# Kernel tuning notes

Hardware: AMD Instinct MI355X
Metric: run time of the kernel (lower is better)

## Reference

```python
import jax, jax.numpy as jnp
import numpy as np

NUM_HEADS = 16
KV_CHANNELS = 128
MASK_FILL = -10000.0  # TE attention_mask_func fill value


def setup_inputs() -> dict:
    key = jax.random.key(0)
    k1, k2, k3 = jax.random.split(key, 3)
    S, B, H = 2048, 2, 2048
    hidden_states = jax.random.normal(k1, (S, B, H), dtype=jnp.float32)
    attention_mask = jnp.zeros((B, 1, S, S), dtype=bool)  # True = masked out
    qkv_weight = jax.random.normal(k2, (H, 3 * H), dtype=jnp.float32) * (1.0 / np.sqrt(H))
    qkv_bias = jnp.zeros((3 * H,), dtype=jnp.float32)
    proj_weight = jax.random.normal(k3, (H, H), dtype=jnp.float32) * (1.0 / np.sqrt(H))
    proj_bias = jnp.zeros((H,), dtype=jnp.float32)
    return {
        "hidden_states": hidden_states,
        "attention_mask": attention_mask,
        "qkv_weight": qkv_weight,
        "qkv_bias": qkv_bias,
        "proj_weight": proj_weight,
        "proj_bias": proj_bias,
    }


def reference(hidden_states, attention_mask, qkv_weight, qkv_bias, proj_weight, proj_bias):
    S, B, H = hidden_states.shape
    nh, d = NUM_HEADS, KV_CHANNELS
    # QKV GEMM: [s,b,H] @ [H,3H] -> [s,b,3H] -> [s,b,nh,3d] -> split
    mixed = hidden_states @ qkv_weight + qkv_bias
    mixed = mixed.reshape(S, B, nh, 3 * d)
    q, k, v = jnp.split(mixed, 3, axis=-1)  # each [s,b,nh,d]
    # BMM1 with 1/sqrt(d) scaling (layer_number=None -> no layer scaling)
    norm_factor = jnp.asarray(np.sqrt(d), dtype=hidden_states.dtype)
    scores = jnp.einsum("sbhd,tbhd->bhst", q, k) / norm_factor  # [b,nh,s,s]
    # causal mask (future positions masked) OR'd with provided bool padding mask
    causal = ~jnp.tril(jnp.ones((S, S), dtype=bool))  # True above diagonal
    mask = jnp.logical_or(causal[None, None], attention_mask)
    scores = jnp.where(mask, jnp.asarray(MASK_FILL, scores.dtype), scores)
    probs = jax.nn.softmax(scores, axis=-1)
    # dropout is identity in eval mode (training=False)
    # BMM2: [b,nh,s,t] x [t,b,nh,d] -> [s,b,nh,d] -> [s,b,H]
    context = jnp.einsum("bhst,tbhd->sbhd", probs, v).reshape(S, B, H)
    # output projection; TE Dense(use_bias=False, return_bias=True) returns bias
    out = context @ proj_weight
    return out, proj_bias
```

## Files before the change

kernel.cpp:

```cpp
#include <hip/hip_runtime.h>
#include <cstdint>
#include <math.h>

#define S_LEN 2048
#define BATCH 2
#define HID   2048
#define NHEAD 16
#define DHEAD 128

typedef _Float16 h8 __attribute__((ext_vector_type(8)));
typedef _Float16 h4 __attribute__((ext_vector_type(4)));
typedef float f32x4 __attribute__((ext_vector_type(4)));

__device__ __forceinline__ void gload16(const void* g, void* l) {
  __builtin_amdgcn_global_load_lds(
      (const __attribute__((address_space(1))) unsigned int*)g,
      (__attribute__((address_space(3))) unsigned int*)l, 16, 0, 0);
}

template <bool HAS_BIAS, bool OUT_HALF>
__global__ __launch_bounds__(512) void gemm_128(
    const _Float16* __restrict__ A, const _Float16* __restrict__ Bt,
    const float* __restrict__ bias, void* __restrict__ Cout, int M, int N,
    int K) {
  __shared__ _Float16 LA[2][8192];
  __shared__ _Float16 LB[2][16384];
  const int tid = (int)threadIdx.x;
  const int wave = tid >> 6, lane = tid & 63;
  const int ln = lane & 15, quad = lane >> 4;
  const int wm = wave >> 2, wn = wave & 3;
  const int bm = (int)blockIdx.y * 128, bn = (int)blockIdx.x * 256;
  const int NT = K >> 6;

  const int gc8 = ((lane & 7) ^ (lane >> 3)) * 8;
  const uint32_t oA0 =
      (uint32_t)(bm + wave * 8 + (lane >> 3)) * (uint32_t)K + (uint32_t)gc8;
  const uint32_t oA1 = oA0 + (uint32_t)(64 * K);
  const uint32_t oB00 =
      (uint32_t)(bn + wave * 16 + (lane >> 3)) * (uint32_t)K + (uint32_t)gc8;
  const uint32_t oB01 = oB00 + (uint32_t)(8 * K);
  const uint32_t oB10 = oB00 + (uint32_t)(128 * K);
  const uint32_t oB11 = oB10 + (uint32_t)(8 * K);

#define STAGE128(bb_, u_)                                                    \
  {                                                                          \
    gload16(A + (oA0 + (uint32_t)(u_)*64u), &LA[bb_][wave * 512]);           \
    gload16(A + (oA1 + (uint32_t)(u_)*64u), &LA[bb_][4096 + wave * 512]);    \
    gload16(Bt + (oB00 + (uint32_t)(u_)*64u), &LB[bb_][wave * 1024]);        \
    gload16(Bt + (oB01 + (uint32_t)(u_)*64u), &LB[bb_][wave * 1024 + 512]);  \
    gload16(Bt + (oB10 + (uint32_t)(u_)*64u), &LB[bb_][8192 + wave * 1024]); \
    gload16(Bt + (oB11 + (uint32_t)(u_)*64u),                                \
            &LB[bb_][8192 + wave * 1024 + 512]);                             \
  }

  const int arow = ln * 64;
  const int sc0 = ((quad ^ (ln & 7))) * 8;
  const int sc1 = (((4 + quad) ^ (ln & 7))) * 8;
  const int abase = wm * 4096;
  const int bbase = wn * 4096;

  f32x4 acc[4][4];
#pragma unroll
  for (int m = 0; m < 4; m++)
#pragma unroll
    for (int n = 0; n < 4; n++) acc[m][n] = (f32x4){0.f, 0.f, 0.f, 0.f};
  h8 aF[4][2], bF[4][2];

#define HQUAD(n0_)                                                           \
  _Pragma("unroll") for (int mm_ = 0; mm_ < 4; mm_++)                        \
      _Pragma("unroll") for (int nn_ = 0; nn_ < 2; nn_++) {                  \
    acc[mm_][(n0_) + nn_] = __builtin_amdgcn_mfma_f32_16x16x32_f16(          \
        aF[mm_][0], bF[(n0_) + nn_][0], acc[mm_][(n0_) + nn_], 0, 0, 0);     \
    acc[mm_][(n0_) + nn_] = __builtin_amdgcn_mfma_f32_16x16x32_f16(          \
        aF[mm_][1], bF[(n0_) + nn_][1], acc[mm_][(n0_) + nn_], 0, 0, 0);     \
  }

  STAGE128(0, 0)
  STAGE128(1, 1)
  asm volatile("s_waitcnt vmcnt(6)" ::: "memory");
  __builtin_amdgcn_s_barrier();

  for (int u = 0; u < NT; ++u) {
    const int bb = u & 1;

#pragma unroll
    for (int m = 0; m < 4; m++) {
      aF[m][0] = *(const h8*)&LA[bb][abase + m * 1024 + arow + sc0];
      aF[m][1] = *(const h8*)&LA[bb][abase + m * 1024 + arow + sc1];
    }
#pragma unroll
    for (int n = 0; n < 2; n++) {
      bF[n][0] = *(const h8*)&LB[bb][bbase + n * 1024 + arow + sc0];
      bF[n][1] = *(const h8*)&LB[bb][bbase + n * 1024 + arow + sc1];
    }
    __builtin_amdgcn_s_barrier();
    __builtin_amdgcn_s_setprio(1);
    HQUAD(0)
    __builtin_amdgcn_s_setprio(0);
    __builtin_amdgcn_s_barrier();

#pragma unroll
    for (int n = 2; n < 4; n++) {
      bF[n][0] = *(const h8*)&LB[bb][bbase + n * 1024 + arow + sc0];
      bF[n][1] = *(const h8*)&LB[bb][bbase + n * 1024 + arow + sc1];
    }
    if (u + 2 < NT) {
      STAGE128(bb, u + 2)
      asm volatile("s_waitcnt vmcnt(6)" ::: "memory");
    } else if (u + 1 < NT) {
      asm volatile("s_waitcnt vmcnt(0)" ::: "memory");
    }
    __builtin_amdgcn_s_barrier();
    __builtin_amdgcn_s_setprio(1);
    HQUAD(2)
    __builtin_amdgcn_s_setprio(0);
    __builtin_amdgcn_s_barrier();
  }
#undef HQUAD
#undef STAGE128

#pragma unroll
  for (int m = 0; m < 4; m++) {
#pragma unroll
    for (int r = 0; r < 4; r++) {
      const size_t row = (size_t)(bm + wm * 64 + m * 16 + quad * 4 + r);
#pragma unroll
      for (int n = 0; n < 4; n++) {
        const int col = bn + wn * 64 + n * 16 + ln;
        float v = acc[m][n][r];
        if (HAS_BIAS) v += bias[col];
        if (OUT_HALF)
          ((_Float16*)Cout)[row * N + col] = (_Float16)v;
        else
          ((float*)Cout)[row * N + col] = v;
      }
    }
  }
}

__global__ __launch_bounds__(256) void transpose_cvt(
    const float* __restrict__ in, _Float16* __restrict__ out, int K, int N) {
  __shared__ float t[64][65];
  const int bn = blockIdx.x * 64, bk = blockIdx.y * 64;
  const int tid = (int)threadIdx.x;
  {
    const int r0 = tid >> 4, c4 = (tid & 15) * 4;
#pragma unroll
    for (int i = 0; i < 4; i++) {
      const int r = r0 + 16 * i;
      float4 v = *(const float4*)&in[(size_t)(bk + r) * N + bn + c4];
      t[r][c4] = v.x;
      t[r][c4 + 1] = v.y;
      t[r][c4 + 2] = v.z;
      t[r][c4 + 3] = v.w;
    }
  }
  __syncthreads();
  {
    const int c0 = tid >> 4, r4 = (tid & 15) * 4;
#pragma unroll
    for (int i = 0; i < 4; i++) {
      const int c = c0 + 16 * i;
      h4 o = {(_Float16)t[r4][c], (_Float16)t[r4 + 1][c],
              (_Float16)t[r4 + 2][c], (_Float16)t[r4 + 3][c]};
      *(h4*)&out[(size_t)(bn + c) * K + bk + r4] = o;
    }
  }
}

__global__ __launch_bounds__(256) void cvt_fp16(const float* __restrict__ in,
                                                _Float16* __restrict__ out,
                                                int n4) {
  int i = blockIdx.x * blockDim.x + threadIdx.x;
  if (i < n4) {
    float4 v = ((const float4*)in)[i];
    h4 o = {(_Float16)v.x, (_Float16)v.y, (_Float16)v.z, (_Float16)v.w};
    *(h4*)&out[4 * (size_t)i] = o;
  }
}

__global__ __launch_bounds__(256) void pack_mask(
    const unsigned char* __restrict__ m, uint32_t* __restrict__ pm) {
  const int i = blockIdx.x * 256 + threadIdx.x;
  const int w = i & 63, r = (i >> 6) & (S_LEN - 1), b = i >> 17;
  const uint32_t* src =
      (const uint32_t*)(m + ((size_t)b * S_LEN + r) * S_LEN + w * 32);
  uint32_t bits = 0;
#pragma unroll
  for (int k = 0; k < 8; k++) {
    const uint32_t v = src[k];
    bits |= ((v & 0x000000FFu) ? 1u : 0u) << (4 * k);
    bits |= ((v & 0x0000FF00u) ? 1u : 0u) << (4 * k + 1);
    bits |= ((v & 0x00FF0000u) ? 1u : 0u) << (4 * k + 2);
    bits |= ((v & 0xFF000000u) ? 1u : 0u) << (4 * k + 3);
  }
  const int c0 = w * 32;
  uint32_t caus;
  if (c0 > r) {
    caus = 0xFFFFFFFFu;
  } else if (r - c0 >= 31) {
    caus = 0u;
  } else {
    caus = ~((2u << (r - c0)) - 1u);
  }
  pm[i] = bits | caus;
}

__global__ __launch_bounds__(256) void pack_kv(
    const _Float16* __restrict__ mixed, _Float16* __restrict__ KP,
    _Float16* __restrict__ VP) {
  __shared__ _Float16 Tv[128 * 40];
  const int kt = blockIdx.x;
  const int z = blockIdx.y;
  const int kb = kt * 32;
  const int tid = threadIdx.x;
  const size_t RS = (size_t)BATCH * NHEAD * 384;
  const _Float16* base = mixed + (size_t)z * 384;

  {
    const int r = tid >> 3, d0 = (tid & 7) * 16;
    const _Float16* src = base + (size_t)(kb + r) * RS + 256 + d0;
    h8 v0 = *(const h8*)src;
    h8 v1 = *(const h8*)(src + 8);
#pragma unroll
    for (int e = 0; e < 8; e++) Tv[(d0 + e) * 40 + r] = v0[e];
#pragma unroll
    for (int e = 0; e < 8; e++) Tv[(d0 + 8 + e) * 40 + r] = v1[e];
  }
  __syncthreads();

  const size_t tb = ((size_t)z * 64 + kt) * 8 * 512;
#pragma unroll
  for (int c = 0; c < 2; c++) {
    const int idx = tid + 256 * c;
    const int i = idx >> 6, l = idx & 63;
    const int ln = l & 15, quad = l >> 4;
    {
      const int jn = i >> 2, kq = i & 3;
      h8 v = *(const h8*)(base + (size_t)(kb + 16 * jn + ln) * RS + 128 +
                          32 * kq + 8 * quad);
      *(h8*)&KP[tb + (size_t)i * 512 + l * 8] = v;
    }
    {
      h8 v = *(const h8*)&Tv[(16 * i + ln) * 40 + 8 * quad];
      *(h8*)&VP[tb + (size_t)i * 512 + l * 8] = v;
    }
  }
}

__global__ __launch_bounds__(512) void flash_attn_v9(
    const _Float16* __restrict__ mixed, const _Float16* __restrict__ KP,
    const _Float16* __restrict__ VP, const uint32_t* __restrict__ pmask,
    _Float16* __restrict__ ctx) {
  const int bid = (int)blockIdx.x;
  const int x = bid & 7, s = bid >> 3;
  const int z = x * 4 + (s & 3);
  const int qt = 15 - (s >> 2);
  const int h = z & (NHEAD - 1), b = z >> 4;
  const int qb = qt * 128;
  const int tid = threadIdx.x;
  const int wave = tid >> 6, lane = tid & 63;
  const int ln = lane & 15, quad = lane >> 4;

  __shared__ _Float16 Kbuf[2][8 * 512];
  __shared__ _Float16 Vbuf[2][8 * 512];
  __shared__ _Float16 St[8][16 * 40];

  const size_t RS = (size_t)BATCH * NHEAD * 384;
  const _Float16* base = mixed + (size_t)z * 384;
  const uint32_t* pmb = pmask + (size_t)b * S_LEN * 64;
  const float scale = 0.08838834764831845f;

  h8 qfrag[4];
  {
    const size_t row = (size_t)(qb + 16 * wave + ln);
#pragma unroll
    for (int kq = 0; kq < 4; kq++) {
      h8 v = *(const h8*)(base + row * RS + 32 * kq + 8 * quad);
#pragma unroll
      for (int j = 0; j < 8; j++) v[j] = (_Float16)((float)v[j] * scale);
      qfrag[kq] = v;
    }
  }

  f32x4 o[8];
#pragma unroll
  for (int nt = 0; nt < 8; nt++) o[nt] = (f32x4){0.f, 0.f, 0.f, 0.f};
  float lpart[4] = {0.f, 0.f, 0.f, 0.f};

  const int ntiles = 4 * qt + 4;

  const size_t zt = (size_t)z * 64;
#define STAGE(kt_, buf_)                                            \
  {                                                                 \
    const size_t tbk = (zt + (kt_)) * (8 * 512) + lane * 8;         \
    gload16(KP + tbk + wave * 512, &Kbuf[buf_][wave * 512]);        \
    gload16(VP + tbk + wave * 512, &Vbuf[buf_][wave * 512]);        \
  }

  STAGE(0, 0)

  const uint32_t* pmr = pmb + (size_t)(qb + 16 * wave + 4 * quad) * 64;

  for (int kt = 0; kt < ntiles; kt++) {
    const int cur = kt & 1;
    __syncthreads();

    if (kt + 1 < ntiles) STAGE(kt + 1, cur ^ 1)

    uint32_t mw[4];
#pragma unroll
    for (int r = 0; r < 4; r++) mw[r] = pmr[(size_t)r * 64 + kt];

    f32x4 sreg[2];
    sreg[0] = (f32x4){0.f, 0.f, 0.f, 0.f};
    sreg[1] = (f32x4){0.f, 0.f, 0.f, 0.f};
#pragma unroll
    for (int kq = 0; kq < 4; kq++) {
#pragma unroll
      for (int jn = 0; jn < 2; jn++) {
        h8 bk = *(const h8*)&Kbuf[cur][(jn * 4 + kq) * 512 + lane * 8];
        sreg[jn] = __builtin_amdgcn_mfma_f32_16x16x32_f16(qfrag[kq], bk,
                                                          sreg[jn], 0, 0, 0);
      }
    }

#pragma unroll
    for (int r = 0; r < 4; r++) {
      const uint32_t ms = mw[r] >> ln;
#pragma unroll
      for (int jn = 0; jn < 2; jn++) {
        const float sv =
            ((ms >> (16 * jn)) & 1u) ? -10000.0f : sreg[jn][r];
        const float p = __expf(sv);
        lpart[r] += p;
        St[wave][(4 * quad + r) * 40 + 16 * jn + ln] = (_Float16)p;
      }
    }
    __threadfence_block();

    {
      h8 ap = *(const h8*)&St[wave][ln * 40 + 8 * quad];
#pragma unroll
      for (int nt = 0; nt < 8; nt++) {
        h8 bv = *(const h8*)&Vbuf[cur][nt * 512 + lane * 8];
        o[nt] = __builtin_amdgcn_mfma_f32_16x16x32_f16(ap, bv, o[nt], 0, 0, 0);
      }
    }
  }
#undef STAGE

#pragma unroll
  for (int r = 0; r < 4; r++) {
    float l = lpart[r];
#pragma unroll
    for (int off = 8; off >= 1; off >>= 1) l += __shfl_xor(l, off, 16);
    const float inv_l = 1.0f / l;
    const size_t row_g = (size_t)(qb + 16 * wave + 4 * quad + r);
    _Float16* dst = ctx + (row_g * BATCH + b) * HID + h * DHEAD;
#pragma unroll
    for (int nt = 0; nt < 8; nt++)
      dst[16 * nt + ln] = (_Float16)(o[nt][r] * inv_l);
  }
}

__global__ void copy_bias(const float* __restrict__ src,
                          float* __restrict__ dst) {
  int i = blockIdx.x * blockDim.x + threadIdx.x;
  if (i < HID) dst[i] = src[i];
}

extern "C" void kernel_launch(void* const* d_in, const int* in_sizes, int n_in,
                              void* d_out, int out_size, void* d_ws,
                              size_t ws_size, hipStream_t stream) {
  (void)in_sizes;
  (void)n_in;
  const float* hs = (const float*)d_in[0];
  const unsigned char* mask = (const unsigned char*)d_in[1];
  const float* qkv_w = (const float*)d_in[2];
  const float* qkv_b = (const float*)d_in[3];
  const float* proj_w = (const float*)d_in[4];
  const float* proj_b = (const float*)d_in[5];
  float* out = (float*)d_out;

  const size_t M = (size_t)S_LEN * BATCH;
  const size_t mixed_e = M * 3 * HID;
  const size_t qkvwt_e = (size_t)3 * HID * HID;
  const size_t hsh_e = M * HID;
  const size_t projwt_e = (size_t)HID * HID;
  const size_t ctx_e = M * HID;
  const size_t need =
      (mixed_e + qkvwt_e + hsh_e + projwt_e + ctx_e) * sizeof(_Float16);
  if (ws_size < need) return;

  _Float16* mixed = (_Float16*)d_ws;
  _Float16* qkv_wt = mixed + mixed_e;
  _Float16* hs_h = qkv_wt + qkvwt_e;
  _Float16* proj_wt = hs_h + hsh_e;
  _Float16* ctx = proj_wt + projwt_e;
  _Float16* KP = hs_h;
  _Float16* VP = qkv_wt;
  uint32_t* pmask = (uint32_t*)out;

  cvt_fp16<<<(int)(hsh_e / 4 / 256), 256, 0, stream>>>(hs, hs_h,
                                                       (int)(hsh_e / 4));
  transpose_cvt<<<dim3(3 * HID / 64, HID / 64), 256, 0, stream>>>(
      qkv_w, qkv_wt, HID, 3 * HID);
  transpose_cvt<<<dim3(HID / 64, HID / 64), 256, 0, stream>>>(
      proj_w, proj_wt, HID, HID);
  pack_mask<<<(BATCH * S_LEN * 64) / 256, 256, 0, stream>>>(mask, pmask);

  gemm_128<true, true><<<dim3(3 * HID / 256, M / 128), 512, 0, stream>>>(
      hs_h, qkv_wt, qkv_b, mixed, (int)M, 3 * HID, HID);

  pack_kv<<<dim3(S_LEN / 32, BATCH * NHEAD), 256, 0, stream>>>(mixed, KP, VP);

  flash_attn_v9<<<512, 512, 0, stream>>>(mixed, KP, VP, pmask, ctx);

  gemm_128<false, false><<<dim3(HID / 256, M / 128), 512, 0, stream>>>(
      ctx, proj_wt, nullptr, out, (int)M, HID, HID);

  copy_bias<<<(HID + 255) / 256, 256, 0, stream>>>(proj_b, out + M * HID);
}
```

Before: 417.7 us.

## Process two 16-row query sub-tiles per wave in flash attention, halving waves

The attention kernel now runs 4 waves per block instead of 8, and each wave handles 32 query rows (two 16-row MFMA tiles) that share every K and V fragment read from LDS. The aim is to halve LDS reads of K/V per MFMA and cut per-block sync overhead. In exchange each wave holds twice the accumulators and Q fragments, which raises register pressure, and there are fewer waves available to hide latency.

```diff
diff --git a/kernel.cpp b/kernel.cpp
--- a/kernel.cpp
+++ b/kernel.cpp
@@ -248,7 +248,7 @@
   }
 }
 
-__global__ __launch_bounds__(512) void flash_attn_v9(
+__global__ __launch_bounds__(256) void flash_attn_v10(
     const _Float16* __restrict__ mixed, const _Float16* __restrict__ KP,
     const _Float16* __restrict__ VP, const uint32_t* __restrict__ pmask,
     _Float16* __restrict__ ctx) {
@@ -264,43 +264,49 @@
 
   __shared__ _Float16 Kbuf[2][8 * 512];
   __shared__ _Float16 Vbuf[2][8 * 512];
-  __shared__ _Float16 St[8][16 * 40];
+  __shared__ _Float16 St[4][32 * 40];
 
   const size_t RS = (size_t)BATCH * NHEAD * 384;
   const _Float16* base = mixed + (size_t)z * 384;
   const uint32_t* pmb = pmask + (size_t)b * S_LEN * 64;
   const float scale = 0.08838834764831845f;
 
-  h8 qfrag[4];
-  {
-    const size_t row = (size_t)(qb + 16 * wave + ln);
+  h8 qfrag[2][4];
+#pragma unroll
+  for (int p = 0; p < 2; p++) {
+    const size_t row = (size_t)(qb + 32 * wave + 16 * p + ln);
 #pragma unroll
     for (int kq = 0; kq < 4; kq++) {
       h8 v = *(const h8*)(base + row * RS + 32 * kq + 8 * quad);
 #pragma unroll
       for (int j = 0; j < 8; j++) v[j] = (_Float16)((float)v[j] * scale);
-      qfrag[kq] = v;
-    }
-  }
-
-  f32x4 o[8];
-#pragma unroll
-  for (int nt = 0; nt < 8; nt++) o[nt] = (f32x4){0.f, 0.f, 0.f, 0.f};
-  float lpart[4] = {0.f, 0.f, 0.f, 0.f};
+      qfrag[p][kq] = v;
+    }
+  }
+
+  f32x4 o[2][8];
+#pragma unroll
+  for (int p = 0; p < 2; p++)
+#pragma unroll
+    for (int nt = 0; nt < 8; nt++) o[p][nt] = (f32x4){0.f, 0.f, 0.f, 0.f};
+  float lpart[2][4] = {{0.f, 0.f, 0.f, 0.f}, {0.f, 0.f, 0.f, 0.f}};
 
   const int ntiles = 4 * qt + 4;
 
   const size_t zt = (size_t)z * 64;
-#define STAGE(kt_, buf_)                                            \
-  {                                                                 \
-    const size_t tbk = (zt + (kt_)) * (8 * 512) + lane * 8;         \
-    gload16(KP + tbk + wave * 512, &Kbuf[buf_][wave * 512]);        \
-    gload16(VP + tbk + wave * 512, &Vbuf[buf_][wave * 512]);        \
+#define STAGE(kt_, buf_)                                                   \
+  {                                                                        \
+    const size_t tbk = (zt + (kt_)) * (8 * 512) + lane * 8;                \
+    _Pragma("unroll") for (int c = 0; c < 2; c++) {                        \
+      const int ch = 2 * wave + c;                                         \
+      gload16(KP + tbk + ch * 512, &Kbuf[buf_][ch * 512]);                 \
+      gload16(VP + tbk + ch * 512, &Vbuf[buf_][ch * 512]);                 \
+    }                                                                      \
   }
 
   STAGE(0, 0)
 
-  const uint32_t* pmr = pmb + (size_t)(qb + 16 * wave + 4 * quad) * 64;
+  const uint32_t* pmr = pmb + (size_t)(qb + 32 * wave + 4 * quad) * 64;
 
   for (int kt = 0; kt < ntiles; kt++) {
     const int cur = kt & 1;
@@ -308,60 +314,76 @@
 
     if (kt + 1 < ntiles) STAGE(kt + 1, cur ^ 1)
 
-    uint32_t mw[4];
-#pragma unroll
-    for (int r = 0; r < 4; r++) mw[r] = pmr[(size_t)r * 64 + kt];
-
-    f32x4 sreg[2];
-    sreg[0] = (f32x4){0.f, 0.f, 0.f, 0.f};
-    sreg[1] = (f32x4){0.f, 0.f, 0.f, 0.f};
+    uint32_t mw[2][4];
+#pragma unroll
+    for (int p = 0; p < 2; p++)
+#pragma unroll
+      for (int r = 0; r < 4; r++)
+        mw[p][r] = pmr[(size_t)(16 * p + r) * 64 + kt];
+
+    f32x4 sp[2][2];
+#pragma unroll
+    for (int p = 0; p < 2; p++)
+#pragma unroll
+      for (int jn = 0; jn < 2; jn++) sp[p][jn] = (f32x4){0.f, 0.f, 0.f, 0.f};
 #pragma unroll
     for (int kq = 0; kq < 4; kq++) {
 #pragma unroll
       for (int jn = 0; jn < 2; jn++) {
         h8 bk = *(const h8*)&Kbuf[cur][(jn * 4 + kq) * 512 + lane * 8];
-        sreg[jn] = __builtin_amdgcn_mfma_f32_16x16x32_f16(qfrag[kq], bk,
-                                                          sreg[jn], 0, 0, 0);
+        sp[0][jn] = __builtin_amdgcn_mfma_f32_16x16x32_f16(qfrag[0][kq], bk,
+                                                           sp[0][jn], 0, 0, 0);
+        sp[1][jn] = __builtin_amdgcn_mfma_f32_16x16x32_f16(qfrag[1][kq], bk,
+                                                           sp[1][jn], 0, 0, 0);
       }
     }
 
 #pragma unroll
-    for (int r = 0; r < 4; r++) {
-      const uint32_t ms = mw[r] >> ln;
-#pragma unroll
-      for (int jn = 0; jn < 2; jn++) {
-        const float sv =
-            ((ms >> (16 * jn)) & 1u) ? -10000.0f : sreg[jn][r];
-        const float p = __expf(sv);
-        lpart[r] += p;
-        St[wave][(4 * quad + r) * 40 + 16 * jn + ln] = (_Float16)p;
+    for (int p = 0; p < 2; p++)
+#pragma unroll
+      for (int r = 0; r < 4; r++) {
+        const uint32_t ms = mw[p][r] >> ln;
+#pragma unroll
+        for (int jn = 0; jn < 2; jn++) {
+          const float sv =
+              ((ms >> (16 * jn)) & 1u) ? -10000.0f : sp[p][jn][r];
+          const float pe = __expf(sv);
+          lpart[p][r] += pe;
+          St[wave][(16 * p + 4 * quad + r) * 40 + 16 * jn + ln] =
+              (_Float16)pe;
+        }
       }
-    }
     __threadfence_block();
 
     {
-      h8 ap = *(const h8*)&St[wave][ln * 40 + 8 * quad];
+      h8 ap0 = *(const h8*)&St[wave][ln * 40 + 8 * quad];
+      h8 ap1 = *(const h8*)&St[wave][(16 + ln) * 40 + 8 * quad];
 #pragma unroll
       for (int nt = 0; nt < 8; nt++) {
         h8 bv = *(const h8*)&Vbuf[cur][nt * 512 + lane * 8];
-        o[nt] = __builtin_amdgcn_mfma_f32_16x16x32_f16(ap, bv, o[nt], 0, 0, 0);
+        o[0][nt] =
+            __builtin_amdgcn_mfma_f32_16x16x32_f16(ap0, bv, o[0][nt], 0, 0, 0);
+        o[1][nt] =
+            __builtin_amdgcn_mfma_f32_16x16x32_f16(ap1, bv, o[1][nt], 0, 0, 0);
       }
     }
   }
 #undef STAGE
 
 #pragma unroll
-  for (int r = 0; r < 4; r++) {
-    float l = lpart[r];
-#pragma unroll
-    for (int off = 8; off >= 1; off >>= 1) l += __shfl_xor(l, off, 16);
-    const float inv_l = 1.0f / l;
-    const size_t row_g = (size_t)(qb + 16 * wave + 4 * quad + r);
-    _Float16* dst = ctx + (row_g * BATCH + b) * HID + h * DHEAD;
-#pragma unroll
-    for (int nt = 0; nt < 8; nt++)
-      dst[16 * nt + ln] = (_Float16)(o[nt][r] * inv_l);
-  }
+  for (int p = 0; p < 2; p++)
+#pragma unroll
+    for (int r = 0; r < 4; r++) {
+      float l = lpart[p][r];
+#pragma unroll
+      for (int off = 8; off >= 1; off >>= 1) l += __shfl_xor(l, off, 16);
+      const float inv_l = 1.0f / l;
+      const size_t row_g = (size_t)(qb + 32 * wave + 16 * p + 4 * quad + r);
+      _Float16* dst = ctx + (row_g * BATCH + b) * HID + h * DHEAD;
+#pragma unroll
+      for (int nt = 0; nt < 8; nt++)
+        dst[16 * nt + ln] = (_Float16)(o[p][nt][r] * inv_l);
+    }
 }
 
 __global__ void copy_bias(const float* __restrict__ src,
@@ -415,7 +437,7 @@
 
   pack_kv<<<dim3(S_LEN / 32, BATCH * NHEAD), 256, 0, stream>>>(mixed, KP, VP);
 
-  flash_attn_v9<<<512, 512, 0, stream>>>(mixed, KP, VP, pmask, ctx);
+  flash_attn_v10<<<512, 256, 0, stream>>>(mixed, KP, VP, pmask, ctx);
 
   gemm_128<false, false><<<dim3(HID / 256, M / 128), 512, 0, stream>>>(
       ctx, proj_wt, nullptr, out, (int)M, HID, HID);
```

After: 426.7 us. +2.2%, slower.
